# Kernel tuning notes

Measured on AMD Instinct MI355X. Metric: run time of the kernel, lower is better.

Reference implementation:

```python
import jax, jax.numpy as jnp
import numpy as np

B, S, E, H = 8, 1024, 512, 8
NEG = -1e10


def setup_inputs() -> dict:
    key = jax.random.key(0)
    ks = jax.random.split(key, 8)
    k = jax.random.normal(ks[0], (B, S, E), dtype=jnp.float32)
    v = jax.random.normal(ks[1], (B, S, E), dtype=jnp.float32)
    q = jax.random.normal(ks[2], (B, S, E), dtype=jnp.float32)
    # causal mask, broadcastable like torch masked_fill
    mask = jnp.tril(jnp.ones((S, S), dtype=jnp.int32))[None, None]
    sc = 1.0 / np.sqrt(E)
    Wk = jax.random.normal(ks[3], (H * E, E), dtype=jnp.float32) * sc
    Wq = jax.random.normal(ks[4], (H * E, E), dtype=jnp.float32) * sc
    Wv = jax.random.normal(ks[5], (H * E, E), dtype=jnp.float32) * sc
    Wo = jax.random.normal(ks[6], (E, H * E), dtype=jnp.float32) * (1.0 / np.sqrt(H * E))
    bo = jnp.zeros((E,), dtype=jnp.float32)
    return {"k": k, "v": v, "q": q, "mask": mask,
            "Wk": Wk, "Wq": Wq, "Wv": Wv, "Wo": Wo, "bo": bo}


def reference(k, v, q, mask, Wk, Wq, Wv, Wo, bo):
    b, q_len, e = q.shape
    k_len, v_len = k.shape[1], v.shape[1]
    h = Wk.shape[0] // e
    scale = jnp.sqrt(jnp.asarray(e // h, dtype=jnp.float32))
    # projections E -> H*E (torch Linear: x @ W.T)
    wk = (k @ Wk.T).reshape(b, h, k_len, e)   # raw reshape, matches torch .view
    wq = (q @ Wq.T).reshape(b, h, q_len, e)
    wv = (v @ Wv.T).reshape(b, h, v_len, e)
    energy = jnp.einsum('bhqe,bhke->bhqk', wq, wk)
    energy = jnp.where(mask == 0, NEG, energy)  # mask applied BEFORE scaling, as in source
    energy = energy / scale
    attn = jax.nn.softmax(energy, axis=-1)
    f = jnp.einsum('bhqk,bhke->bhqe', attn, wv)
    f = jnp.transpose(f, (0, 2, 1, 3)).reshape(b, q_len, h * e)
    return f @ Wo.T + bo
```

## Files before the change

### kernel.cpp

```cpp
#include <hip/hip_runtime.h>


typedef _Float16 half8 __attribute__((ext_vector_type(8)));
typedef _Float16 half4v __attribute__((ext_vector_type(4)));
typedef float f32x4 __attribute__((ext_vector_type(4)));

typedef __attribute__((address_space(3))) unsigned int lds_u32_t;
typedef __attribute__((address_space(1))) unsigned int g_u32_t;

__device__ __forceinline__ void glds16(const void* g, void* l) {
  __builtin_amdgcn_global_load_lds((const g_u32_t*)g, (lds_u32_t*)l, 16, 0, 0);
}

__device__ __forceinline__ void stage_panel(const _Float16* __restrict__ G,
                                            int ld, _Float16* Ls, int tid) {
  int w = tid >> 6;
#pragma unroll
  for (int e = 0; e < 2; e++) {
    int X = e * 8192 + tid * 16;
    int r = X >> 6;
    int s = (X >> 4) & 3;
    glds16(G + (size_t)r * ld + ((s ^ (r & 3)) << 3),
           Ls + ((e * 8192 + w * 1024) >> 1));
  }
}

template <int NT>
__device__ __forceinline__ void gemm256_core(const _Float16* __restrict__ A,
                                             const _Float16* __restrict__ B,
                                             int lda, int ldb,
                                             _Float16* smem, f32x4 (&acc)[8][4]) {
  int tid = (int)threadIdx.x;
  int w = tid >> 6, lane = tid & 63;
  int wr = (w >> 2) * 128, wc = (w & 3) * 64;
  int lr = lane & 15;
  int sw = ((lane >> 4) ^ (lane & 3)) << 3;

#pragma unroll
  for (int t = 0; t < 3; t++) {
    if (t < NT) {
      stage_panel(A + t * 32, lda, smem + t * 16384, tid);
      stage_panel(B + t * 32, ldb, smem + t * 16384 + 8192, tid);
    }
  }
  for (int t = 0; t < NT; t++) {
    if (t + 3 < NT) {
      _Float16* buf = smem + ((t + 3) & 3) * 16384;
      stage_panel(A + (t + 3) * 32, lda, buf, tid);
      stage_panel(B + (t + 3) * 32, ldb, buf + 8192, tid);
    }
    int ahead = NT - 1 - t;
    if (ahead > 3) ahead = 3;
    if (ahead == 3)      asm volatile("s_waitcnt vmcnt(12)" ::: "memory");
    else if (ahead == 2) asm volatile("s_waitcnt vmcnt(8)" ::: "memory");
    else if (ahead == 1) asm volatile("s_waitcnt vmcnt(4)" ::: "memory");
    else                 asm volatile("s_waitcnt vmcnt(0)" ::: "memory");
    __builtin_amdgcn_s_barrier();
    __builtin_amdgcn_sched_barrier(0);
    const _Float16* As = smem + (t & 3) * 16384;
    const _Float16* Bs = As + 8192;
    half8 a[8], b[4];
#pragma unroll
    for (int ni = 0; ni < 4; ni++)
      b[ni] = *(const half8*)&Bs[(wc + ni * 16 + lr) * 32 + sw];
#pragma unroll
    for (int mi = 0; mi < 8; mi++)
      a[mi] = *(const half8*)&As[(wr + mi * 16 + lr) * 32 + sw];
    __builtin_amdgcn_s_setprio(1);
#pragma unroll
    for (int mi = 0; mi < 8; mi++)
#pragma unroll
      for (int ni = 0; ni < 4; ni++)
        acc[mi][ni] = __builtin_amdgcn_mfma_f32_16x16x32_f16(a[mi], b[ni],
                                                             acc[mi][ni], 0, 0, 0);
    __builtin_amdgcn_s_setprio(0);
    __builtin_amdgcn_sched_barrier(0);
    __builtin_amdgcn_s_barrier();
  }
}

__device__ __forceinline__ void epilogue256(f32x4 (&acc)[8][4], _Float16* lds,
                                            _Float16* Cp, size_t cOff,
                                            int i0, int j0, int ldc) {
  int tid = (int)threadIdx.x;
  int w = tid >> 6, lane = tid & 63;
  int wr = (w >> 2) * 128, wc = (w & 3) * 64;
  int r0 = (lane >> 4) * 4, cl = lane & 15;
  _Float16* T = lds + w * 8192;
#pragma unroll
  for (int mi = 0; mi < 8; mi++)
#pragma unroll
    for (int ni = 0; ni < 4; ni++) {
      int colb = ni * 16 + cl;
#pragma unroll
      for (int r = 0; r < 4; r++) {
        int row = mi * 16 + r0 + r;
        T[row * 64 + ((((colb >> 3) ^ row) & 7) << 3) + (colb & 7)] =
            (_Float16)acc[mi][ni][r];
      }
    }
#pragma unroll
  for (int st = 0; st < 16; st++) {
    int row = st * 8 + (lane >> 3);
    int c8 = lane & 7;
    half8 h = *(const half8*)&T[row * 64 + (((c8 ^ row) & 7) << 3)];
    *(half8*)(Cp + cOff + (size_t)(i0 + wr + row) * ldc + j0 + wc + c8 * 8) = h;
  }
}

template <int HG>
__global__ __launch_bounds__(512, 2) void proj256(const _Float16* __restrict__ in16,
                                                  const _Float16* __restrict__ W16,
                                                  _Float16* __restrict__ Qp,
                                                  _Float16* __restrict__ Kp,
                                                  _Float16* __restrict__ Vp) {
  __shared__ __align__(16) _Float16 smem[65536];
  int x = (int)blockIdx.x, Y = (int)blockIdx.y;
  int it = x >> 4, jt = x & 15;
  const _Float16* A = in16 + (size_t)Y * HG * 524288 + (size_t)it * 131072;
  const _Float16* B = W16 + (size_t)Y * 2097152 + (size_t)jt * 131072;
  _Float16* C = (Y == 0 ? Qp : (Y == 1 ? Kp : Vp));
  f32x4 acc[8][4] = {};
  gemm256_core<16>(A, B, 512, 512, smem, acc);
  epilogue256(acc, smem, C, 0, it * 256, jt * 256, 4096);
}

template <int HG>
__global__ __launch_bounds__(512, 2) void vwo256(const _Float16* __restrict__ Vp,
                                                 const _Float16* __restrict__ WoG,
                                                 _Float16* __restrict__ VWo) {
  __shared__ __align__(16) _Float16 smem[65536];
  int x = (int)blockIdx.x, Y = (int)blockIdx.y, Z = (int)blockIdx.z;
  size_t z = (size_t)Z * HG + Y;
  int i0 = (x >> 2) * 256, j0 = (x & 3) * 256;
  const _Float16* A = WoG + (size_t)Y * 512 + (size_t)i0 * 4096;
  const _Float16* B = Vp + z * 524288 + (size_t)j0 * 512;
  f32x4 acc[8][4] = {};
  gemm256_core<16>(A, B, 4096, 512, smem, acc);
  epilogue256(acc, smem, VWo, z * 524288, i0, j0, 1024);
}

template <int HG>
__global__ __launch_bounds__(512, 2) void energy256(const _Float16* __restrict__ Qp,
                                                    const _Float16* __restrict__ Kp,
                                                    _Float16* __restrict__ E) {
  __shared__ __align__(16) _Float16 smem[65536];
  int x = (int)blockIdx.x, Y = (int)blockIdx.y, Z = (int)blockIdx.z;
  size_t z = (size_t)Z * HG + Y;
  int ti = (int)((sqrtf(8.0f * x + 1.0f) - 1.0f) * 0.5f);
  if (ti * (ti + 1) / 2 > x) ti--;
  else if ((ti + 1) * (ti + 2) / 2 <= x) ti++;
  int tj = x - ti * (ti + 1) / 2;
  int i0 = ti * 256, j0 = tj * 256;
  const _Float16* A = Qp + z * 524288 + (size_t)i0 * 512;
  const _Float16* B = Kp + z * 524288 + (size_t)j0 * 512;
  f32x4 acc[8][4] = {};
  gemm256_core<16>(A, B, 512, 512, smem, acc);
  epilogue256(acc, smem, E, z * 1048576, i0, j0, 1024);
}

template <int HL>
__device__ __forceinline__ void gemm_core(const _Float16* A, const _Float16* B,
                                          int lda, int ldb, int kmax,
                                          long sAh, long sBh,
                                          _Float16* As, _Float16* Bs,
                                          f32x4 (&acc)[4][4]) {
  int tid = (int)threadIdx.x;
  int w = tid >> 6, lane = tid & 63;
  int wr = (w >> 1) * 64, wc = (w & 1) * 64;
  int lr = lane & 15, lk = (lane >> 4) * 8;
  int srow = lane >> 2, sseg = (lane & 3) * 8;

  for (int h = 0; h < HL; h++) {
    const _Float16* Ah = A + (size_t)h * sAh;
    const _Float16* Bh = B + (size_t)h * sBh;
    for (int k0 = 0; k0 < kmax; k0 += 64) {
      __syncthreads();
#pragma unroll
      for (int p = 0; p < 2; p++)
#pragma unroll
        for (int t = 0; t < 2; t++) {
          glds16(Ah + (size_t)(w * 32 + t * 16 + srow) * lda + k0 + p * 32 + sseg,
                 As + p * 4096 + (w * 32 + t * 16) * 32);
          glds16(Bh + (size_t)(w * 32 + t * 16 + srow) * ldb + k0 + p * 32 + sseg,
                 Bs + p * 4096 + (w * 32 + t * 16) * 32);
        }
      __syncthreads();
#pragma unroll
      for (int p = 0; p < 2; p++) {
        half8 a[4], b[4];
#pragma unroll
        for (int mi = 0; mi < 4; mi++)
          a[mi] = *(half8*)&As[p * 4096 + (wr + mi * 16 + lr) * 32 + lk];
#pragma unroll
        for (int ni = 0; ni < 4; ni++)
          b[ni] = *(half8*)&Bs[p * 4096 + (wc + ni * 16 + lr) * 32 + lk];
#pragma unroll
        for (int mi = 0; mi < 4; mi++)
#pragma unroll
          for (int ni = 0; ni < 4; ni++)
            acc[mi][ni] =
                __builtin_amdgcn_mfma_f32_16x16x32_f16(a[mi], b[ni], acc[mi][ni], 0, 0, 0);
      }
    }
  }
}

__device__ __forceinline__ void epilogue_atomic(f32x4 (&acc)[4][4], float* Cp,
                                                size_t cOff, int i0, int j0, int ldc) {
  int tid = (int)threadIdx.x;
  int w = tid >> 6, lane = tid & 63;
  int wr = (w >> 1) * 64, wc = (w & 1) * 64;
  int r0 = (lane >> 4) * 4, col = lane & 15;
#pragma unroll
  for (int mi = 0; mi < 4; mi++)
#pragma unroll
    for (int ni = 0; ni < 4; ni++)
#pragma unroll
      for (int r = 0; r < 4; r++)
        unsafeAtomicAdd(Cp + cOff + (size_t)(i0 + wr + mi * 16 + r0 + r) * ldc +
                            j0 + wc + ni * 16 + col,
                        acc[mi][ni][r]);
}

template <int HG, int HL>
__global__ __launch_bounds__(256) void pv_kernel(const _Float16* __restrict__ E,
                                                 const _Float16* __restrict__ VWo,
                                                 float* __restrict__ out) {
  __shared__ __align__(16) _Float16 smem[17408];
  int x = (int)blockIdx.x, Y = (int)blockIdx.y, Z = (int)blockIdx.z;
  int i0 = (x >> 2) * 128, j0 = (x & 3) * 128;
  int kmax = i0 + 128;
  const _Float16* A = E + ((size_t)Z * HG + (size_t)Y * HL) * 1048576 + (size_t)i0 * 1024;
  const _Float16* B = VWo + ((size_t)Z * HG + (size_t)Y * HL) * 524288 + (size_t)j0 * 1024;
  f32x4 acc[4][4] = {};
  gemm_core<HL>(A, B, 1024, 1024, kmax, 1048576, 524288, smem, smem + 8192, acc);
  epilogue_atomic(acc, out, (size_t)Z * 524288, i0, j0, 512);
}

__global__ __launch_bounds__(256) void softmax_rows(void* __restrict__ Ep) {
  int R = (int)blockIdx.x * 4 + ((int)threadIdx.x >> 6);
  int lane = (int)threadIdx.x & 63;
  int i = R & 1023;
  int nt = (i >> 8) + 1;
  _Float16* row = (_Float16*)Ep + (size_t)R * 1024;
  float x[16];
  float m = -3.0e38f;
#pragma unroll
  for (int t = 0; t < 4; t++) {
    if (t < nt) {
      int j0 = t * 256 + lane * 4;
      half4v h = *(const half4v*)(row + j0);
#pragma unroll
      for (int c = 0; c < 4; c++) {
        float v = (j0 + c <= i) ? (float)h[c] * 0.125f : -3.0e38f;
        x[t * 4 + c] = v;
        m = fmaxf(m, v);
      }
    }
  }
#pragma unroll
  for (int s = 32; s > 0; s >>= 1) m = fmaxf(m, __shfl_xor(m, s, 64));
  float p[16];
  float sum = 0.0f;
#pragma unroll
  for (int t = 0; t < 4; t++) {
    if (t < nt) {
#pragma unroll
      for (int c = 0; c < 4; c++) {
        p[t * 4 + c] = exp2f((x[t * 4 + c] - m) * 1.44269504f);
        sum += p[t * 4 + c];
      }
    }
  }
#pragma unroll
  for (int s = 32; s > 0; s >>= 1) sum += __shfl_xor(sum, s, 64);
  float inv = 1.0f / sum;
#pragma unroll
  for (int t = 0; t < 4; t++) {
    if (t < nt) {
      int j0 = t * 256 + lane * 4;
      half4v h;
#pragma unroll
      for (int c = 0; c < 4; c++) h[c] = (_Float16)(p[t * 4 + c] * inv);
      *(half4v*)(row + j0) = h;
    }
  }
}

__global__ __launch_bounds__(256) void wbconv(const float* __restrict__ Wq,
                                              const float* __restrict__ Wk,
                                              const float* __restrict__ Wv,
                                              const float* __restrict__ Wo,
                                              _Float16* __restrict__ W16,
                                              float* __restrict__ out,
                                              const float* __restrict__ bo) {
  int bx = (int)blockIdx.x;
  if (bx < 4096) {
    size_t base = ((size_t)bx * 256 + threadIdx.x) * 8;
    int wid = (int)(base >> 21);
    size_t off = base & 2097151;
    const float* src = wid == 0 ? Wq : (wid == 1 ? Wk : (wid == 2 ? Wv : Wo));
    float4 a = *(const float4*)(src + off);
    float4 b = *(const float4*)(src + off + 4);
    half8 h;
    h[0] = (_Float16)a.x; h[1] = (_Float16)a.y; h[2] = (_Float16)a.z; h[3] = (_Float16)a.w;
    h[4] = (_Float16)b.x; h[5] = (_Float16)b.y; h[6] = (_Float16)b.z; h[7] = (_Float16)b.w;
    *(half8*)(W16 + base) = h;
  } else {
    size_t idx = ((size_t)(bx - 4096) * 256 + threadIdx.x) * 4;
    *(float4*)(out + idx) = *(const float4*)(bo + (idx & 511));
  }
}

template <int HG>
__global__ __launch_bounds__(256) void inconv(const float* __restrict__ q,
                                              const float* __restrict__ k,
                                              const float* __restrict__ v,
                                              _Float16* __restrict__ dst) {
  int Y = (int)blockIdx.y;
  size_t base = ((size_t)blockIdx.x * 256 + threadIdx.x) * 8;
  size_t b = base / (HG * 65536);
  size_t within = base - b * (HG * 65536);
  const float* src = (Y == 0 ? q : (Y == 1 ? k : v)) + b * 524288 + within;
  float4 a = ((const float4*)src)[0];
  float4 c = ((const float4*)src)[1];
  half8 h;
  h[0] = (_Float16)a.x; h[1] = (_Float16)a.y; h[2] = (_Float16)a.z; h[3] = (_Float16)a.w;
  h[4] = (_Float16)c.x; h[5] = (_Float16)c.y; h[6] = (_Float16)c.z; h[7] = (_Float16)c.w;
  *(half8*)(dst + (size_t)Y * HG * 524288 + base) = h;
}

template <int HG>
static void run_pipeline(const float* q_in, const float* k_in, const float* v_in,
                         const float* Wq, const float* Wk, const float* Wv,
                         const float* Wo, const float* bo, float* out, char* ws,
                         hipStream_t stream) {
  const int NG = 8 / HG;
  const long zc = 8 * HG;
  _Float16* W16 = (_Float16*)ws;
  _Float16* in16 = W16 + 8388608;
  _Float16* Qp = in16 + 3L * HG * 524288;
  _Float16* Kp = Qp + zc * 524288;
  _Float16* VWo = Kp + zc * 524288;
  _Float16* E = VWo + zc * 524288;
  _Float16* Vp = E;
  _Float16* Wo16 = W16 + 3 * 2097152;
  dim3 blk(256);
  dim3 blk5(512);

  wbconv<<<dim3(8192), blk, 0, stream>>>(Wq, Wk, Wv, Wo, W16, out, bo);

  constexpr int HL = (HG >= 2) ? 2 : 1;
  constexpr int YS = HG / HL;

  for (int g = 0; g < NG; g++) {
    inconv<HG><<<dim3(HG * 256, 3), blk, 0, stream>>>(
        q_in + (size_t)g * HG * 65536, k_in + (size_t)g * HG * 65536,
        v_in + (size_t)g * HG * 65536, in16);

    proj256<HG><<<dim3(HG * 64, 3), blk5, 0, stream>>>(in16, W16, Qp, Kp, Vp);

    vwo256<HG><<<dim3(8, HG, 8), blk5, 0, stream>>>(
        Vp, Wo16 + (size_t)g * HG * 512, VWo);

    energy256<HG><<<dim3(10, HG, 8), blk5, 0, stream>>>(Qp, Kp, E);

    softmax_rows<<<dim3(zc * 256), blk, 0, stream>>>(E);

    pv_kernel<HG, HL><<<dim3(32, YS, 8), blk, 0, stream>>>(E, VWo, out);
  }
}

extern "C" void kernel_launch(void* const* d_in, const int* in_sizes, int n_in,
                              void* d_out, int out_size, void* d_ws, size_t ws_size,
                              hipStream_t stream) {
  const float* k_in = (const float*)d_in[0];
  const float* v_in = (const float*)d_in[1];
  const float* q_in = (const float*)d_in[2];
  const float* Wk = (const float*)d_in[4];
  const float* Wq = (const float*)d_in[5];
  const float* Wv = (const float*)d_in[6];
  const float* Wo = (const float*)d_in[7];
  const float* bo = (const float*)d_in[8];
  float* out = (float*)d_out;
  char* ws = (char*)d_ws;

  if (ws_size >= (size_t)197132288)
    run_pipeline<4>(q_in, k_in, v_in, Wq, Wk, Wv, Wo, bo, out, ws, stream);
  else if (ws_size >= (size_t)106954752)
    run_pipeline<2>(q_in, k_in, v_in, Wq, Wk, Wv, Wo, bo, out, ws, stream);
  else
    run_pipeline<1>(q_in, k_in, v_in, Wq, Wk, Wv, Wo, bo, out, ws, stream);
}
```

Before: 566.8 us.

## Switch 256-tile GEMM core to double-buffered 64-wide K panels with split MFMA phases

The 256x256 GEMM core used by the projection, VWo and energy kernels changes from a 4-stage ring of 32-wide K panels to a 2-stage double buffer of 64-wide K panels. The next panel's load is issued right after the barrier. Each K step is split into phases: A fragments are loaded in two halves of 4 rows, with barriers and lgkmcnt waits between the MFMA groups, which cuts register pressure and interleaves LDS reads with compute. The aim is fewer barriers per K and fewer live A registers. The cost is a shallower prefetch depth, and each step now waits for vmcnt(0), which may expose global-load latency.

```diff
diff --git a/kernel.cpp b/kernel.cpp
--- a/kernel.cpp
+++ b/kernel.cpp
@@ -12,15 +12,15 @@
   __builtin_amdgcn_global_load_lds((const g_u32_t*)g, (lds_u32_t*)l, 16, 0, 0);
 }
 
-__device__ __forceinline__ void stage_panel(const _Float16* __restrict__ G,
-                                            int ld, _Float16* Ls, int tid) {
+__device__ __forceinline__ void stage_panel64(const _Float16* __restrict__ G,
+                                              int ld, _Float16* Ls, int tid) {
   int w = tid >> 6;
 #pragma unroll
-  for (int e = 0; e < 2; e++) {
+  for (int e = 0; e < 4; e++) {
     int X = e * 8192 + tid * 16;
-    int r = X >> 6;
-    int s = (X >> 4) & 3;
-    glds16(G + (size_t)r * ld + ((s ^ (r & 3)) << 3),
+    int r = X >> 7;
+    int s = (X >> 4) & 7;
+    glds16(G + (size_t)r * ld + (((s ^ (r & 7)) & 7) << 3),
            Ls + ((e * 8192 + w * 1024) >> 1));
   }
 }
@@ -33,50 +33,64 @@
   int tid = (int)threadIdx.x;
   int w = tid >> 6, lane = tid & 63;
   int wr = (w >> 2) * 128, wc = (w & 3) * 64;
-  int lr = lane & 15;
-  int sw = ((lane >> 4) ^ (lane & 3)) << 3;
-
-#pragma unroll
-  for (int t = 0; t < 3; t++) {
-    if (t < NT) {
-      stage_panel(A + t * 32, lda, smem + t * 16384, tid);
-      stage_panel(B + t * 32, ldb, smem + t * 16384 + 8192, tid);
-    }
-  }
+  int lr = lane & 15, hi = lane >> 4, l7 = lane & 7;
+
+  stage_panel64(A, lda, smem, tid);
+  stage_panel64(B, ldb, smem + 16384, tid);
+
   for (int t = 0; t < NT; t++) {
-    if (t + 3 < NT) {
-      _Float16* buf = smem + ((t + 3) & 3) * 16384;
-      stage_panel(A + (t + 3) * 32, lda, buf, tid);
-      stage_panel(B + (t + 3) * 32, ldb, buf + 8192, tid);
-    }
-    int ahead = NT - 1 - t;
-    if (ahead > 3) ahead = 3;
-    if (ahead == 3)      asm volatile("s_waitcnt vmcnt(12)" ::: "memory");
-    else if (ahead == 2) asm volatile("s_waitcnt vmcnt(8)" ::: "memory");
-    else if (ahead == 1) asm volatile("s_waitcnt vmcnt(4)" ::: "memory");
-    else                 asm volatile("s_waitcnt vmcnt(0)" ::: "memory");
+    asm volatile("s_waitcnt vmcnt(0)" ::: "memory");
     __builtin_amdgcn_s_barrier();
     __builtin_amdgcn_sched_barrier(0);
-    const _Float16* As = smem + (t & 3) * 16384;
-    const _Float16* Bs = As + 8192;
-    half8 a[8], b[4];
-#pragma unroll
-    for (int ni = 0; ni < 4; ni++)
-      b[ni] = *(const half8*)&Bs[(wc + ni * 16 + lr) * 32 + sw];
-#pragma unroll
-    for (int mi = 0; mi < 8; mi++)
-      a[mi] = *(const half8*)&As[(wr + mi * 16 + lr) * 32 + sw];
-    __builtin_amdgcn_s_setprio(1);
-#pragma unroll
-    for (int mi = 0; mi < 8; mi++)
+    if (t + 1 < NT) {
+      _Float16* nb = smem + ((t + 1) & 1) * 32768;
+      stage_panel64(A + (t + 1) * 64, lda, nb, tid);
+      stage_panel64(B + (t + 1) * 64, ldb, nb + 16384, tid);
+    }
+    const _Float16* As = smem + (t & 1) * 32768;
+    const _Float16* Bs = As + 16384;
+    half8 a[4], b[4];
+#pragma unroll
+    for (int ks = 0; ks < 2; ks++) {
+      int seg = (((ks * 4 + hi) ^ l7) & 7) << 3;
 #pragma unroll
       for (int ni = 0; ni < 4; ni++)
-        acc[mi][ni] = __builtin_amdgcn_mfma_f32_16x16x32_f16(a[mi], b[ni],
-                                                             acc[mi][ni], 0, 0, 0);
-    __builtin_amdgcn_s_setprio(0);
-    __builtin_amdgcn_sched_barrier(0);
-    __builtin_amdgcn_s_barrier();
-  }
+        b[ni] = *(const half8*)&Bs[(wc + ni * 16 + lr) * 64 + seg];
+#pragma unroll
+      for (int mi = 0; mi < 4; mi++)
+        a[mi] = *(const half8*)&As[(wr + mi * 16 + lr) * 64 + seg];
+      __builtin_amdgcn_sched_barrier(0);
+      __builtin_amdgcn_s_barrier();
+      asm volatile("s_waitcnt lgkmcnt(0)" ::: "memory");
+      __builtin_amdgcn_sched_barrier(0);
+      __builtin_amdgcn_s_setprio(1);
+#pragma unroll
+      for (int mi = 0; mi < 4; mi++)
+#pragma unroll
+        for (int ni = 0; ni < 4; ni++)
+          acc[mi][ni] = __builtin_amdgcn_mfma_f32_16x16x32_f16(a[mi], b[ni],
+                                                               acc[mi][ni], 0, 0, 0);
+      __builtin_amdgcn_s_setprio(0);
+      __builtin_amdgcn_sched_barrier(0);
+#pragma unroll
+      for (int mi = 0; mi < 4; mi++)
+        a[mi] = *(const half8*)&As[(wr + (mi + 4) * 16 + lr) * 64 + seg];
+      __builtin_amdgcn_sched_barrier(0);
+      __builtin_amdgcn_s_barrier();
+      asm volatile("s_waitcnt lgkmcnt(0)" ::: "memory");
+      __builtin_amdgcn_sched_barrier(0);
+      __builtin_amdgcn_s_setprio(1);
+#pragma unroll
+      for (int mi = 0; mi < 4; mi++)
+#pragma unroll
+        for (int ni = 0; ni < 4; ni++)
+          acc[mi + 4][ni] = __builtin_amdgcn_mfma_f32_16x16x32_f16(a[mi], b[ni],
+                                                                   acc[mi + 4][ni], 0, 0, 0);
+      __builtin_amdgcn_s_setprio(0);
+      __builtin_amdgcn_sched_barrier(0);
+    }
+  }
+  __syncthreads();
 }
 
 __device__ __forceinline__ void epilogue256(f32x4 (&acc)[8][4], _Float16* lds,
@@ -121,7 +135,7 @@
   const _Float16* B = W16 + (size_t)Y * 2097152 + (size_t)jt * 131072;
   _Float16* C = (Y == 0 ? Qp : (Y == 1 ? Kp : Vp));
   f32x4 acc[8][4] = {};
-  gemm256_core<16>(A, B, 512, 512, smem, acc);
+  gemm256_core<8>(A, B, 512, 512, smem, acc);
   epilogue256(acc, smem, C, 0, it * 256, jt * 256, 4096);
 }
 
@@ -136,7 +150,7 @@
   const _Float16* A = WoG + (size_t)Y * 512 + (size_t)i0 * 4096;
   const _Float16* B = Vp + z * 524288 + (size_t)j0 * 512;
   f32x4 acc[8][4] = {};
-  gemm256_core<16>(A, B, 4096, 512, smem, acc);
+  gemm256_core<8>(A, B, 4096, 512, smem, acc);
   epilogue256(acc, smem, VWo, z * 524288, i0, j0, 1024);
 }
 
@@ -155,7 +169,7 @@
   const _Float16* A = Qp + z * 524288 + (size_t)i0 * 512;
   const _Float16* B = Kp + z * 524288 + (size_t)j0 * 512;
   f32x4 acc[8][4] = {};
-  gemm256_core<16>(A, B, 512, 512, smem, acc);
+  gemm256_core<8>(A, B, 512, 512, smem, acc);
   epilogue256(acc, smem, E, z * 1048576, i0, j0, 1024);
 }
 
```

Result: faster. 530.1 us (-6.5%).
